# Performance work log

Hardware: AMD Instinct MI355X
Metric: run time of the kernel (lower is better)

Reference implementation:

```python
import jax, jax.numpy as jnp
import numpy as np

N, M, BS = 32, 64, 512
ALPHA, BETA = 1.0, 1.0


def setup_inputs() -> dict:
    key = jax.random.key(0)
    k1, k2, k3, k4 = jax.random.split(key, 4)
    q = jax.random.normal(k1, (BS, N), jnp.float32)
    b = jax.random.normal(k2, (BS, M), jnp.float32)
    A0 = jax.random.normal(k3, (N, N), jnp.float32)
    P = A0 @ A0.T / N + jnp.eye(N, dtype=jnp.float32)  # SPD cost matrix
    H = jax.random.normal(k4, (M, N), jnp.float32) / jnp.sqrt(jnp.float32(N))
    return {"q": q, "b": b, "P": P, "H": H, "iters": 1000}


def reference(q, b, P, H, iters):
    m = H.shape[0]
    # Pinv-applied quantities via solve (matches torch.linalg.solve / pinv usage)
    Pinv_q = jnp.linalg.solve(P, q.T).T                 # (bs, n)
    D = H @ jnp.linalg.solve(P, H.T)                    # (m, m) = H P^-1 H^T
    # dummy preconditioner: scaled identity keeping the operator nonexpansive
    lam_max = jnp.linalg.eigvalsh(D)[-1]
    tD = (BETA / lam_max) * jnp.eye(m, dtype=q.dtype)   # (m, m)
    mu = ((H @ Pinv_q.T).T - b) @ tD.T                  # (bs, m)
    tDD = tD @ D
    I = jnp.eye(m, dtype=q.dtype)
    A = jnp.block([[tDD, tD],
                   [-2.0 * ALPHA * tDD + I, I - 2.0 * ALPHA * tD]])  # (2m, 2m)
    B = jnp.concatenate([mu, -2.0 * ALPHA * mu], axis=1)             # (bs, 2m)
    Hinv = jnp.linalg.pinv(H)                            # (n, m)
    X0 = jnp.zeros((q.shape[0], 2 * m), q.dtype)

    def step(X, _):
        X = X @ A.T + B
        X = X.at[:, m:].set(jax.nn.relu(X[:, m:]))       # in-place ReLU on dual half
        return X, X

    _, ys = jax.lax.scan(step, X0, None, length=iters)   # (iters, bs, 2m)
    Xs = jnp.concatenate([X0[None], ys], axis=0).transpose(1, 0, 2)  # (bs, iters+1, 2m)
    # primal_sols[k] = Hinv @ (X_k[m:] - b)
    primal_sols = jnp.einsum('nm,bkm->bkn', Hinv, Xs[:, :, m:] - b[:, None, :])
    return Xs, primal_sols
```

## Files before the change

### kernel.cpp

```cpp
#include <hip/hip_runtime.h>
#include <math.h>

#define BATCH 512
#define ITERS 1000
#define PLEN 25
#define PHASES 40

typedef float f32x2 __attribute__((ext_vector_type(2)));
typedef float f32x4 __attribute__((ext_vector_type(4)));

__device__ __forceinline__ float rdlane(float v, int l) {
  return __int_as_float(__builtin_amdgcn_readlane(__float_as_int(v), l));
}
__device__ __forceinline__ f32x2 fma2(f32x2 a, f32x2 b, f32x2 c) {
#if __has_builtin(__builtin_elementwise_fma)
  return __builtin_elementwise_fma(a, b, c);
#else
  f32x2 r; r.x = fmaf(a.x, b.x, c.x); r.y = fmaf(a.y, b.y, c.y); return r;
#endif
}

#define GJ32_REG(g)                                            \
  _Pragma("unroll")                                            \
  for (int k = 0; k < 32; ++k) {                               \
    float inv = 1.0f / rdlane(g[k], k);                        \
    g[k] *= inv;                                               \
    _Pragma("unroll")                                          \
    for (int ii = 0; ii < 32; ++ii) {                          \
      if (ii == k) continue;                                   \
      float f = rdlane(g[ii], k);                              \
      g[ii] = fmaf(-f, g[k], g[ii]);                           \
    }                                                          \
  }

__global__ __launch_bounds__(128, 1)
void fused_kernel(const float* __restrict__ q,
                  const float* __restrict__ bmat,
                  const float* __restrict__ P,
                  const float* __restrict__ H,
                  float* __restrict__ Xs,
                  float* __restrict__ out2) {
  __shared__ __align__(16) float stage[2112];
  __shared__ __align__(16) float X1R[2][PLEN][64];
  __shared__ __align__(16) float X2R[2][PLEN][64];

  const int tid = threadIdx.x;
  const int wv = tid >> 6;
  const int lane = tid & 63;
  const int row = blockIdx.x;
  const int i = lane & 31, h = lane >> 5;

  float hreg[32];
  {
    const f32x4* hp = (const f32x4*)(H + lane * 32);
    #pragma unroll
    for (int j4 = 0; j4 < 8; ++j4) {
      f32x4 t = hp[j4];
      hreg[4*j4+0] = t.x; hreg[4*j4+1] = t.y; hreg[4*j4+2] = t.z; hreg[4*j4+3] = t.w;
    }
  }
  const float bl = bmat[row * 64 + lane];

  float dcol[64]; float s = 0.f, mu = 0.f;
  f32x2 hv2[16];
  float* Xp = Xs + (size_t)row * (ITERS + 1) * 128;
  float* ob = out2 + (size_t)row * (ITERS + 1) * 32;

  if (wv == 1) {
    #pragma unroll
    for (int j = 0; j < 32; ++j) stage[lane * 33 + j] = hreg[j];
  }
  __syncthreads();
  float gB[32];
  if (wv == 1) {
    float htc[64];
    #pragma unroll
    for (int m = 0; m < 64; ++m) htc[m] = stage[m * 33 + i];
    #pragma unroll
    for (int r = 0; r < 32; ++r) {
      float a0 = 0.f, a1 = 0.f;
      #pragma unroll
      for (int m = 0; m < 64; m += 2) {
        a0 = fmaf(rdlane(hreg[r], m),     htc[m],     a0);
        a1 = fmaf(rdlane(hreg[r], m + 1), htc[m + 1], a1);
      }
      float hth = a0 + a1;
      gB[r] = (lane < 32) ? hth : (((lane - 32) == r) ? 1.0f : 0.0f);
    }
    GJ32_REG(gB)
  }
  __syncthreads();
  if (wv == 1) {
    #pragma unroll
    for (int r = 0; r < 32; ++r) {
      float a0 = 0.f, a1 = 0.f;
      #pragma unroll
      for (int c = 0; c < 32; c += 2) {
        a0 = fmaf(rdlane(gB[r], 32 + c),     hreg[c],     a0);
        a1 = fmaf(rdlane(gB[r], 32 + c + 1), hreg[c + 1], a1);
      }
      stage[r * 66 + lane] = a0 + a1;
    }
  }
  __syncthreads();
  if (wv == 1) {
    #pragma unroll
    for (int t = 0; t < 16; ++t)
      hv2[t] = *(const f32x2*)&stage[i * 66 + 32 * h + 2 * t];
  }

  if (wv == 0) {
    float pht[32], acc;
    {
      float g[32];
      #pragma unroll
      for (int r = 0; r < 32; ++r) {
        float pv = P[r * 32 + i];
        g[r] = (lane < 32) ? pv : (((lane - 32) == r) ? 1.0f : 0.0f);
      }
      GJ32_REG(g)
      #pragma unroll
      for (int r = 0; r < 32; ++r) {
        float a0 = 0.f, a1 = 0.f;
        #pragma unroll
        for (int j = 0; j < 32; j += 2) {
          a0 = fmaf(rdlane(g[r], 32 + j),     hreg[j],     a0);
          a1 = fmaf(rdlane(g[r], 32 + j + 1), hreg[j + 1], a1);
        }
        pht[r] = a0 + a1;
      }
    }
    {
      const float* qp = q + row * 32;
      float a0 = 0.f, a1 = 0.f;
      #pragma unroll
      for (int r = 0; r < 32; r += 2) {
        a0 = fmaf(qp[r],     pht[r],     a0);
        a1 = fmaf(qp[r + 1], pht[r + 1], a1);
      }
      acc = a0 + a1;
    }
    #pragma unroll
    for (int r = 0; r < 64; ++r) {
      float a0 = 0.f, a1 = 0.f;
      #pragma unroll
      for (int j = 0; j < 32; j += 2) {
        a0 = fmaf(rdlane(hreg[j],     r), pht[j],     a0);
        a1 = fmaf(rdlane(hreg[j + 1], r), pht[j + 1], a1);
      }
      dcol[r] = a0 + a1;
    }
    {
      float ecol[64];
      #pragma unroll
      for (int r = 0; r < 64; ++r) {
        float a0 = 0.f, a1 = 0.f;
        #pragma unroll
        for (int c = 0; c < 64; c += 2) {
          a0 = fmaf(rdlane(dcol[r], c),     dcol[c],     a0);
          a1 = fmaf(rdlane(dcol[r], c + 1), dcol[c + 1], a1);
        }
        ecol[r] = a0 + a1;
      }
      float v = 1.0f + 0.017f * (float)lane;
      #pragma unroll 1
      for (int t = 0; t < 112; ++t) {
        float a0 = 0.f, a1 = 0.f, a2 = 0.f, a3 = 0.f;
        #pragma unroll
        for (int c = 0; c < 64; c += 4) {
          a0 = fmaf(ecol[c+0], rdlane(v, c+0), a0);
          a1 = fmaf(ecol[c+1], rdlane(v, c+1), a1);
          a2 = fmaf(ecol[c+2], rdlane(v, c+2), a2);
          a3 = fmaf(ecol[c+3], rdlane(v, c+3), a3);
        }
        v = (a0 + a1) + (a2 + a3);
        if ((t & 7) == 7) {
          float n2 = v * v;
          #pragma unroll
          for (int m = 1; m < 64; m <<= 1) n2 += __shfl_xor(n2, m);
          v *= 1.0f / sqrtf(n2);
        }
      }
      float a0 = 0.f, a1 = 0.f, a2 = 0.f, a3 = 0.f;
      #pragma unroll
      for (int c = 0; c < 64; c += 4) {
        a0 = fmaf(dcol[c+0], rdlane(v, c+0), a0);
        a1 = fmaf(dcol[c+1], rdlane(v, c+1), a1);
        a2 = fmaf(dcol[c+2], rdlane(v, c+2), a2);
        a3 = fmaf(dcol[c+3], rdlane(v, c+3), a3);
      }
      float w = (a0 + a1) + (a2 + a3);
      float num = w * v, den = v * v;
      #pragma unroll
      for (int m = 1; m < 64; m <<= 1) {
        num += __shfl_xor(num, m);
        den += __shfl_xor(den, m);
      }
      s = den / num;
    }
    mu = s * (acc - bl);
    #pragma unroll
    for (int r = 0; r < 64; ++r) dcol[r] *= s;
  }

  float x1 = 0.f, x2 = 0.f;
  #pragma unroll 1
  for (int p = 0; p < PHASES; ++p) {
    if (wv == 0) {
      float* rx1 = &X1R[p & 1][0][0];
      float* rx2 = &X2R[p & 1][0][0];
      #pragma unroll 1
      for (int u = 0; u < PLEN; ++u) {
        float a0 = 0.f, a1 = 0.f, a2 = 0.f, a3 = 0.f;
        #pragma unroll
        for (int j8 = 0; j8 < 64; j8 += 8) {
          float b0 = rdlane(x1, j8+0), b1 = rdlane(x1, j8+1);
          float b2 = rdlane(x1, j8+2), b3 = rdlane(x1, j8+3);
          float b4 = rdlane(x1, j8+4), b5 = rdlane(x1, j8+5);
          float b6 = rdlane(x1, j8+6), b7 = rdlane(x1, j8+7);
          a0 = fmaf(dcol[j8+0], b0, a0);
          a1 = fmaf(dcol[j8+1], b1, a1);
          a2 = fmaf(dcol[j8+2], b2, a2);
          a3 = fmaf(dcol[j8+3], b3, a3);
          a0 = fmaf(dcol[j8+4], b4, a0);
          a1 = fmaf(dcol[j8+5], b5, a1);
          a2 = fmaf(dcol[j8+6], b6, a2);
          a3 = fmaf(dcol[j8+7], b7, a3);
        }
        float x1n = ((a0 + a1) + (a2 + a3)) + fmaf(s, x2, mu);
        float x2n = fmaxf(fmaf(-2.0f, x1n, x1 + x2), 0.f);
        rx1[u * 64 + lane] = x1n;
        rx2[u * 64 + lane] = x2n - bl;
        x1 = x1n; x2 = x2n;
      }
    } else {
      if (p == 0) {
        Xp[lane] = 0.f;
        Xp[64 + lane] = 0.f;
        f32x2 pa = {0.f, 0.f}, pb = {0.f, 0.f};
        #pragma unroll
        for (int t = 0; t < 8; ++t) {
          f32x2 ta, tb;
          ta.x = -__shfl(bl, 32*h + 4*t + 0, 64);
          ta.y = -__shfl(bl, 32*h + 4*t + 1, 64);
          tb.x = -__shfl(bl, 32*h + 4*t + 2, 64);
          tb.y = -__shfl(bl, 32*h + 4*t + 3, 64);
          pa = fma2(hv2[2*t],     ta, pa);
          pb = fma2(hv2[2*t + 1], tb, pb);
        }
        float pr = (pa.x + pa.y) + (pb.x + pb.y);
        pr += __shfl_xor(pr, 32);
        if (h == 0) ob[i] = pr;
      } else {
        const float* rx1 = &X1R[(p - 1) & 1][0][0];
        const float* rx2 = &X2R[(p - 1) & 1][0][0];
        const int k0 = PLEN * (p - 1) + 1;
        float* Xk = Xp + (size_t)k0 * 128;
        float* obk = ob + (size_t)k0 * 32;
        #pragma unroll 1
        for (int u = 0; u < PLEN; ++u) {
          float x1v = rx1[u * 64 + lane];
          float x2mb = rx2[u * 64 + lane];
          Xk[u * 128 + lane] = x1v;
          Xk[u * 128 + 64 + lane] = x2mb + bl;
          const f32x4* tp = (const f32x4*)(rx2 + u * 64 + h * 32);
          f32x2 pa = {0.f, 0.f}, pb = {0.f, 0.f};
          #pragma unroll
          for (int t = 0; t < 8; ++t) {
            f32x4 tv = tp[t];
            pa = fma2(hv2[2*t],     tv.xy, pa);
            pb = fma2(hv2[2*t + 1], tv.zw, pb);
          }
          float pr = (pa.x + pa.y) + (pb.x + pb.y);
          pr += __shfl_xor(pr, 32);
          if (h == 0) obk[u * 32 + i] = pr;
        }
      }
    }
    __syncthreads();
  }

  if (wv == 1) {
    const float* rx1 = &X1R[1][0][0];
    const float* rx2 = &X2R[1][0][0];
    const int k0 = PLEN * (PHASES - 1) + 1;
    float* Xk = Xp + (size_t)k0 * 128;
    float* obk = ob + (size_t)k0 * 32;
    #pragma unroll 1
    for (int u = 0; u < PLEN; ++u) {
      float x1v = rx1[u * 64 + lane];
      float x2mb = rx2[u * 64 + lane];
      Xk[u * 128 + lane] = x1v;
      Xk[u * 128 + 64 + lane] = x2mb + bl;
      const f32x4* tp = (const f32x4*)(rx2 + u * 64 + h * 32);
      f32x2 pa = {0.f, 0.f}, pb = {0.f, 0.f};
      #pragma unroll
      for (int t = 0; t < 8; ++t) {
        f32x4 tv = tp[t];
        pa = fma2(hv2[2*t],     tv.xy, pa);
        pb = fma2(hv2[2*t + 1], tv.zw, pb);
      }
      float pr = (pa.x + pa.y) + (pb.x + pb.y);
      pr += __shfl_xor(pr, 32);
      if (h == 0) obk[u * 32 + i] = pr;
    }
  }
}

extern "C" void kernel_launch(void* const* d_in, const int* in_sizes, int n_in,
                              void* d_out, int out_size, void* d_ws, size_t ws_size,
                              hipStream_t stream) {
  (void)in_sizes; (void)n_in; (void)out_size; (void)d_ws; (void)ws_size;
  const float* q = (const float*)d_in[0];
  const float* b = (const float*)d_in[1];
  const float* P = (const float*)d_in[2];
  const float* H = (const float*)d_in[3];
  float* Xs = (float*)d_out;
  float* out2 = Xs + (size_t)BATCH * (ITERS + 1) * 128;

  fused_kernel<<<BATCH, 128, 0, stream>>>(q, b, P, H, Xs, out2);
}
```

Baseline: 611.9 us.

## Pack two batch rows per block with two producer and two consumer waves

Each block now handles two batch rows using four waves: waves 0-1 run the serial recurrence for one row each, and waves 2-3 write Xs and the primal projection for the matching row. The grid is halved to 256 blocks of 256 threads, with shared ring buffers duplicated per row. The goal is to fit all 512 rows onto the mi355x's compute units in a single wave of blocks, so rows are no longer processed in two rounds. Both consumer waves now redo the H^T H inversion redundantly, and the phase barriers couple the two rows.

```diff
diff --git a/kernel.cpp b/kernel.cpp
--- a/kernel.cpp
+++ b/kernel.cpp
@@ -33,7 +33,7 @@
     }                                                          \
   }
 
-__global__ __launch_bounds__(128, 1)
+__global__ __launch_bounds__(256, 1)
 void fused_kernel(const float* __restrict__ q,
                   const float* __restrict__ bmat,
                   const float* __restrict__ P,
@@ -41,13 +41,15 @@
                   float* __restrict__ Xs,
                   float* __restrict__ out2) {
   __shared__ __align__(16) float stage[2112];
-  __shared__ __align__(16) float X1R[2][PLEN][64];
-  __shared__ __align__(16) float X2R[2][PLEN][64];
+  __shared__ __align__(16) float X1R[2][2][PLEN][64];
+  __shared__ __align__(16) float X2R[2][2][PLEN][64];
 
   const int tid = threadIdx.x;
   const int wv = tid >> 6;
   const int lane = tid & 63;
-  const int row = blockIdx.x;
+  const int rib = wv & 1;
+  const bool prod = (wv < 2);
+  const int rg = 2 * blockIdx.x + rib;
   const int i = lane & 31, h = lane >> 5;
 
   float hreg[32];
@@ -59,20 +61,20 @@
       hreg[4*j4+0] = t.x; hreg[4*j4+1] = t.y; hreg[4*j4+2] = t.z; hreg[4*j4+3] = t.w;
     }
   }
-  const float bl = bmat[row * 64 + lane];
+  const float bl = bmat[(size_t)rg * 64 + lane];
 
   float dcol[64]; float s = 0.f, mu = 0.f;
   f32x2 hv2[16];
-  float* Xp = Xs + (size_t)row * (ITERS + 1) * 128;
-  float* ob = out2 + (size_t)row * (ITERS + 1) * 32;
-
-  if (wv == 1) {
+  float* Xp = Xs + (size_t)rg * (ITERS + 1) * 128;
+  float* ob = out2 + (size_t)rg * (ITERS + 1) * 32;
+
+  if (wv == 2) {
     #pragma unroll
     for (int j = 0; j < 32; ++j) stage[lane * 33 + j] = hreg[j];
   }
   __syncthreads();
   float gB[32];
-  if (wv == 1) {
+  if (!prod) {
     float htc[64];
     #pragma unroll
     for (int m = 0; m < 64; ++m) htc[m] = stage[m * 33 + i];
@@ -90,7 +92,7 @@
     GJ32_REG(gB)
   }
   __syncthreads();
-  if (wv == 1) {
+  if (wv == 2) {
     #pragma unroll
     for (int r = 0; r < 32; ++r) {
       float a0 = 0.f, a1 = 0.f;
@@ -103,13 +105,13 @@
     }
   }
   __syncthreads();
-  if (wv == 1) {
+  if (!prod) {
     #pragma unroll
     for (int t = 0; t < 16; ++t)
       hv2[t] = *(const f32x2*)&stage[i * 66 + 32 * h + 2 * t];
   }
 
-  if (wv == 0) {
+  if (prod) {
     float pht[32], acc;
     {
       float g[32];
@@ -131,7 +133,7 @@
       }
     }
     {
-      const float* qp = q + row * 32;
+      const float* qp = q + (size_t)rg * 32;
       float a0 = 0.f, a1 = 0.f;
       #pragma unroll
       for (int r = 0; r < 32; r += 2) {
@@ -206,9 +208,9 @@
   float x1 = 0.f, x2 = 0.f;
   #pragma unroll 1
   for (int p = 0; p < PHASES; ++p) {
-    if (wv == 0) {
-      float* rx1 = &X1R[p & 1][0][0];
-      float* rx2 = &X2R[p & 1][0][0];
+    if (prod) {
+      float* rx1 = &X1R[rib][p & 1][0][0];
+      float* rx2 = &X2R[rib][p & 1][0][0];
       #pragma unroll 1
       for (int u = 0; u < PLEN; ++u) {
         float a0 = 0.f, a1 = 0.f, a2 = 0.f, a3 = 0.f;
@@ -252,8 +254,8 @@
         pr += __shfl_xor(pr, 32);
         if (h == 0) ob[i] = pr;
       } else {
-        const float* rx1 = &X1R[(p - 1) & 1][0][0];
-        const float* rx2 = &X2R[(p - 1) & 1][0][0];
+        const float* rx1 = &X1R[rib][(p - 1) & 1][0][0];
+        const float* rx2 = &X2R[rib][(p - 1) & 1][0][0];
         const int k0 = PLEN * (p - 1) + 1;
         float* Xk = Xp + (size_t)k0 * 128;
         float* obk = ob + (size_t)k0 * 32;
@@ -280,9 +282,9 @@
     __syncthreads();
   }
 
-  if (wv == 1) {
-    const float* rx1 = &X1R[1][0][0];
-    const float* rx2 = &X2R[1][0][0];
+  if (!prod) {
+    const float* rx1 = &X1R[rib][1][0][0];
+    const float* rx2 = &X2R[rib][1][0][0];
     const int k0 = PLEN * (PHASES - 1) + 1;
     float* Xk = Xp + (size_t)k0 * 128;
     float* obk = ob + (size_t)k0 * 32;
@@ -318,5 +320,5 @@
   float* Xs = (float*)d_out;
   float* out2 = Xs + (size_t)BATCH * (ITERS + 1) * 128;
 
-  fused_kernel<<<BATCH, 128, 0, stream>>>(q, b, P, H, Xs, out2);
+  fused_kernel<<<BATCH / 2, 256, 0, stream>>>(q, b, P, H, Xs, out2);
 }
```

After: 619.2 us. About the same (+1.2%).
